# Optimization experiments

Hardware: AMD Instinct MI355X
Metric: run time of the kernel (lower is better)

The kernel has to match this reference:

```python
import jax, jax.numpy as jnp
import numpy as np

EPS = 1e-12  # torch F.normalize eps

def _l2norm(x):
    n = jnp.linalg.norm(x, axis=1, keepdims=True)
    return x / jnp.maximum(n, EPS)

def setup_inputs() -> dict:
    key = jax.random.key(0)
    kq, km = jax.random.split(key)
    queries = jax.random.normal(kq, (4096, 128), dtype=jnp.float32)
    memory = jax.random.normal(km, (100000, 128), dtype=jnp.float32)
    return {"queries": queries, "memory": memory, "k": 3}

def reference(queries, memory, k):
    q = _l2norm(queries)                      # [N, D]
    m = _l2norm(memory)                       # [M, D]
    sims = q @ m.T                            # [N, M]
    values, indices = jax.lax.top_k(sims, k)  # [N, k] each
    distances = 1.0 - values
    return distances, indices
```

## Files before the change

kernel.cpp:

```cpp
#include <hip/hip_runtime.h>
#include <hip/hip_bf16.h>

typedef unsigned short u16;
typedef unsigned int u32;
typedef unsigned long long u64;

#define N_Q 4096
#define N_M 100000
#define N_M_PAD 100096
#define DDIM 128
#define QTILE 256
#define MTILE 64
#define NCHUNK 32
#define NQT (N_Q / QTILE)
#define TOTAL_MT (N_M_PAD / MTILE)
#define TPC ((TOTAL_MT + NCHUNK - 1) / NCHUNK)
#define NCAND (NCHUNK * 2 * 3)

typedef short bf16x8 __attribute__((ext_vector_type(8)));
typedef float f32x4 __attribute__((ext_vector_type(4)));
typedef float f32x16 __attribute__((ext_vector_type(16)));

static __device__ __forceinline__ u16 f2bf(float v) {
  union { float f; u32 u; } a; a.f = v;
  u32 r = a.u + 0x7fffu + ((a.u >> 16) & 1u);
  return (u16)(r >> 16);
}

static __device__ __forceinline__ void async_copy16(const u16* gp, u16* lp) {
  __builtin_amdgcn_global_load_lds(
      (const __attribute__((address_space(1))) u32*)gp,
      (__attribute__((address_space(3))) u32*)lp, 16, 0, 0);
}

static __device__ __forceinline__ int mbcnt64(u64 m) {
  return __builtin_amdgcn_mbcnt_hi((u32)(m >> 32),
                                   __builtin_amdgcn_mbcnt_lo((u32)m, 0));
}

__global__ __launch_bounds__(256) void knorm(const float* __restrict__ q, const float* __restrict__ m,
                                             u16* __restrict__ qn, u16* __restrict__ mn,
                                             float* __restrict__ qinv, float* __restrict__ minv) {
  const int lane = threadIdx.x & 63;
  const int l16 = lane & 15;
  const int sub = lane >> 4;
  const int wgl = blockIdx.x * 4 + (threadIdx.x >> 6);
  const int step = gridDim.x * 16;
  for (int row = wgl * 4 + sub; row < N_Q + N_M_PAD; row += step) {
    const float* src;
    u16* dst;
    int mr = 0;
    bool is_q = (row < N_Q);
    bool pad = false;
    if (is_q) {
      src = q + (size_t)row * DDIM;
      dst = qn + (size_t)row * DDIM;
    } else {
      mr = row - N_Q;
      pad = (mr >= N_M);
      src = m + (size_t)mr * DDIM;
      dst = mn + (size_t)mr * DDIM;
    }
    float4 a, b;
    if (pad) {
      a.x = a.y = a.z = a.w = 0.f;
      b = a;
    } else {
      a = ((const float4*)src)[l16];
      b = ((const float4*)src)[l16 + 16];
    }
    float s = a.x * a.x + a.y * a.y + a.z * a.z + a.w * a.w +
              b.x * b.x + b.y * b.y + b.z * b.z + b.w * b.w;
    #pragma unroll
    for (int off = 1; off < 16; off <<= 1) s += __shfl_xor(s, off, 64);
    float invn = 1.0f / fmaxf(sqrtf(s), 1e-12f);
    u32 p0 = (u32)f2bf(a.x * invn) | ((u32)f2bf(a.y * invn) << 16);
    u32 p1 = (u32)f2bf(a.z * invn) | ((u32)f2bf(a.w * invn) << 16);
    u32 p2 = (u32)f2bf(b.x * invn) | ((u32)f2bf(b.y * invn) << 16);
    u32 p3 = (u32)f2bf(b.z * invn) | ((u32)f2bf(b.w * invn) << 16);
    uint2 w0; w0.x = p0; w0.y = p1;
    uint2 w1; w1.x = p2; w1.y = p3;
    *(uint2*)&dst[l16 * 4] = w0;
    *(uint2*)&dst[64 + l16 * 4] = w1;
    if (l16 == 0) {
      if (is_q) qinv[row] = invn;
      else minv[mr] = pad ? 0.f : invn;
    }
  }
}

static __device__ __forceinline__ void stage2(const u16* __restrict__ mn, u16* dst,
                                              int t, const u32* goff, u32 loff0) {
  const u16* gbase = mn + (size_t)t * MTILE * DDIM;
  #pragma unroll
  for (int it = 0; it < 2; ++it)
    async_copy16(gbase + goff[it], dst + loff0 + (u32)(it * 64) * 8);
}

static __device__ __forceinline__ void tileWork(
    const u16* As, int tl, int wm, int h, int l15, int l31,
    const bf16x8 (&bq)[2][8], float (&tv0)[2], float (&tv1)[2], float (&tv2)[2]) {
  f32x16 acc[2];
  __builtin_amdgcn_s_setprio(1);
  {
    int c = h ^ l15;
    bf16x8 a = *(const bf16x8*)&As[((wm * 32 + l31) * 16 + c) * 8];
    f32x16 z = {0.f,0.f,0.f,0.f,0.f,0.f,0.f,0.f,0.f,0.f,0.f,0.f,0.f,0.f,0.f,0.f};
    acc[0] = __builtin_amdgcn_mfma_f32_32x32x16_bf16(a, bq[0][0], z, 0, 0, 0);
    acc[1] = __builtin_amdgcn_mfma_f32_32x32x16_bf16(a, bq[1][0], z, 0, 0, 0);
  }
  #pragma unroll
  for (int s = 1; s < 8; ++s) {
    int c = (s * 2 + h) ^ l15;
    bf16x8 a = *(const bf16x8*)&As[((wm * 32 + l31) * 16 + c) * 8];
    acc[0] = __builtin_amdgcn_mfma_f32_32x32x16_bf16(a, bq[0][s], acc[0], 0, 0, 0);
    acc[1] = __builtin_amdgcn_mfma_f32_32x32x16_bf16(a, bq[1][s], acc[1], 0, 0, 0);
  }
  __builtin_amdgcn_s_setprio(0);
  const u32 codeBase = ((u32)tl << 2) | ((u32)h << 1);
  #pragma unroll
  for (int ni = 0; ni < 2; ++ni) {
    #pragma unroll
    for (int g = 0; g < 2; ++g) {
      float M = fmaxf(
          fmaxf(fmaxf(acc[ni][g * 8 + 0], acc[ni][g * 8 + 1]),
                fmaxf(acc[ni][g * 8 + 2], acc[ni][g * 8 + 3])),
          fmaxf(fmaxf(acc[ni][g * 8 + 4], acc[ni][g * 8 + 5]),
                fmaxf(acc[ni][g * 8 + 6], acc[ni][g * 8 + 7])));
      float pk = __uint_as_float((__float_as_uint(M) & 0xFFFFFE00u) | (codeBase | (u32)g));
      tv2[ni] = __builtin_amdgcn_fmed3f(tv1[ni], tv2[ni], pk);
      tv1[ni] = __builtin_amdgcn_fmed3f(tv0[ni], tv1[ni], pk);
      tv0[ni] = fmaxf(tv0[ni], pk);
    }
  }
}

__global__ __launch_bounds__(512, 4) void kgemm(const u16* __restrict__ qn,
                                                const u16* __restrict__ mn,
                                                float* __restrict__ pval) {
  __shared__ u16 B0[MTILE * DDIM];
  __shared__ u16 B1[MTILE * DDIM];
  __shared__ u16 B2[MTILE * DDIM];
  __shared__ u16 B3[MTILE * DDIM];

  const int id = blockIdx.x;
  const int xcd = id & 7, sub = id >> 3;
  const int ch = xcd * 4 + (sub >> 4);
  const int qt = sub & 15;
  const int tid = threadIdx.x;
  const int wid = tid >> 6, lane = tid & 63;
  const int l15 = lane & 15, l31 = lane & 31, h = lane >> 5;
  const int wm = wid >> 2, wq = wid & 3;

  const int t0 = ch * TPC;
  const int t1 = (t0 + TPC < TOTAL_MT) ? (t0 + TPC) : TOTAL_MT;
  const int nt = t1 - t0;

  u32 goff[2];
  u32 loff0;
  {
    int u0 = wid * 128 + lane;
    loff0 = (u32)(wid * 128) * 8;
    #pragma unroll
    for (int it = 0; it < 2; ++it) {
      int u = u0 + it * 64;
      int row = u >> 4, su = u & 15;
      int k8 = su ^ (row & 15);
      goff[it] = (u32)(row * DDIM + k8 * 8);
    }
  }

  stage2(mn, B0, t0 + 0, goff, loff0);
  stage2(mn, B1, t0 + 1, goff, loff0);
  stage2(mn, B2, t0 + 2, goff, loff0);

  bf16x8 bq[2][8];
  #pragma unroll
  for (int ni = 0; ni < 2; ++ni) {
    int col = qt * QTILE + wq * 64 + ni * 32 + l31;
    #pragma unroll
    for (int s = 0; s < 8; ++s)
      bq[ni][s] = *(const bf16x8*)&qn[(size_t)col * DDIM + (s * 2 + h) * 8];
  }

  float tv0[2], tv1[2], tv2[2];
  #pragma unroll
  for (int i = 0; i < 2; ++i) { tv0[i] = tv1[i] = tv2[i] = -1e30f; }

  asm volatile("s_waitcnt vmcnt(0)" ::: "memory");
  asm volatile("s_barrier" ::: "memory");

  int r = 0;
  #define ROUND(BC, BS)                                                        \
    {                                                                          \
      int ts = t0 + r + 3;                                                     \
      ts = (ts < t1) ? ts : (t1 - 1);                                          \
      stage2(mn, BS, ts, goff, loff0);                                         \
      tileWork(BC, r, wm, h, l15, l31, bq, tv0, tv1, tv2);                     \
      asm volatile("s_waitcnt vmcnt(4)" ::: "memory");                         \
      asm volatile("s_barrier" ::: "memory");                                  \
      ++r;                                                                     \
      if (r >= nt) break;                                                      \
    }
  while (true) {
    ROUND(B0, B3)
    ROUND(B1, B0)
    ROUND(B2, B1)
    ROUND(B3, B2)
  }
  #undef ROUND

  #pragma unroll
  for (int ni = 0; ni < 2; ++ni) {
    float a0 = tv0[ni], a1 = tv1[ni], a2 = tv2[ni];
    float b0 = __shfl_xor(a0, 32, 64);
    float b1 = __shfl_xor(a1, 32, 64);
    float b2 = __shfl_xor(a2, 32, 64);
    float n0 = fmaxf(a0, b0);
    float n1 = __builtin_amdgcn_fmed3f(a0, b0, fmaxf(a1, b1));
    float n2 = fmaxf(fmaxf(fminf(a1, b0), fminf(a0, b1)), fmaxf(a2, b2));
    int qlocal = wq * 64 + ni * 32 + l31;
    size_t base = (((size_t)qt * NCHUNK + ch) * QTILE + qlocal) * 6 + wm * 3;
    if (h == 0) {
      pval[base] = n0;
      pval[base + 1] = n1;
    } else {
      pval[base + 2] = n2;
    }
  }
}

__global__ __launch_bounds__(256) void kmerge(const float* __restrict__ pval,
                                              const float* __restrict__ q,
                                              const float* __restrict__ mem,
                                              const float* __restrict__ qinv,
                                              const float* __restrict__ minv,
                                              float* __restrict__ out) {
  __shared__ float sv[4][64];
  __shared__ u32 spk[4][8];
  __shared__ u32 spo[4][8];
  const int tid = threadIdx.x;
  const int wq = tid >> 6;
  const int lane = tid & 63;
  const int qg = blockIdx.x * 4 + wq;
  const int qt = qg >> 8, ql = qg & 255;

  const int c0 = lane * 3;
  float cv[3];
  {
    int chn = c0 / 6, rem = c0 - chn * 6;
    size_t b = (((size_t)qt * NCHUNK + chn) * QTILE + ql) * 6 + rem;
    cv[0] = pval[b];
    cv[1] = pval[b + 1];
    cv[2] = pval[b + 2];
  }

  u32 k[3];
  #pragma unroll
  for (int i = 0; i < 3; ++i) {
    u32 u = __float_as_uint(cv[i]);
    k[i] = (u & 0x80000000u) ? ~u : (u | 0x80000000u);
  }

  u32 t = 0;
  #pragma unroll
  for (int b = 31; b >= 0; --b) {
    u32 cand = t | (1u << b);
    int loc = (int)(k[0] >= cand) + (int)(k[1] >= cand) + (int)(k[2] >= cand);
    u64 B0 = __ballot(loc & 1);
    u64 B1 = __ballot(loc & 2);
    int cnt = __popcll(B0) + 2 * __popcll(B1);
    if (cnt >= 8) t = cand;
  }

  {
    u64 G[3], E[3];
    #pragma unroll
    for (int i = 0; i < 3; ++i) {
      G[i] = __ballot(k[i] > t);
      E[i] = __ballot(k[i] == t);
    }
    int c1 = __popcll(G[0]) + __popcll(G[1]) + __popcll(G[2]);
    int bg = mbcnt64(G[0]) + mbcnt64(G[1]) + mbcnt64(G[2]);
    int be = mbcnt64(E[0]) + mbcnt64(E[1]) + mbcnt64(E[2]);
    int og = 0, oe = 0;
    #pragma unroll
    for (int i = 0; i < 3; ++i) {
      int slot = 99;
      if (k[i] > t) { slot = bg + og; ++og; }
      else if (k[i] == t) { slot = c1 + be + oe; ++oe; }
      if (slot < 8) {
        spk[wq][slot] = __float_as_uint(cv[i]);
        spo[wq][slot] = (u32)(c0 + i);
      }
    }
  }
  __syncthreads();

  const float qi = qinv[qg];
  const float* qrow = q + (size_t)qg * DDIM;
  const int e = lane >> 3, f = lane & 7;

  float4 qv[4];
  #pragma unroll
  for (int i = 0; i < 4; ++i) qv[i] = *(const float4*)&qrow[(f + 8 * i) * 4];

  #pragma unroll
  for (int p = 0; p < 8; ++p) {
    int bp = (int)spo[wq][p];
    u32 code = spk[wq][p] & 511u;
    int chn = bp / 6;
    int wm = (bp - chn * 6) / 3;
    int tl = (int)(code >> 2), hh = (int)((code >> 1) & 1u), g = (int)(code & 1u);
    int row = (chn * TPC + tl) * MTILE + wm * 32 + g * 16 + (e >> 2) * 8 + hh * 4 + (e & 3);
    bool valid = (row < N_M);
    int ra = valid ? row : 0;
    const float* mrow = mem + (size_t)ra * DDIM;
    float s = 0.f;
    #pragma unroll
    for (int i = 0; i < 4; ++i) {
      float4 mv = *(const float4*)&mrow[(f + 8 * i) * 4];
      s += qv[i].x * mv.x + qv[i].y * mv.y + qv[i].z * mv.z + qv[i].w * mv.w;
    }
    #pragma unroll
    for (int off = 1; off < 8; off <<= 1) s += __shfl_xor(s, off, 64);
    s = valid ? (s * qi * minv[ra]) : -1e30f;
    if (f == 0) sv[wq][p * 8 + e] = s;
  }
  __syncthreads();

  float myv = sv[wq][lane];
  {
    int p = lane >> 3, e2 = lane & 7;
    int bp = (int)spo[wq][p];
    u32 code = spk[wq][p] & 511u;
    int chn = bp / 6;
    int wm = (bp - chn * 6) / 3;
    int tl = (int)(code >> 2), hh = (int)((code >> 1) & 1u), g = (int)(code & 1u);
    int row = (chn * TPC + tl) * MTILE + wm * 32 + g * 16 + (e2 >> 2) * 8 + hh * 4 + (e2 & 3);
    int myrow = (row < N_M) ? row : (N_M + lane);

    #pragma unroll
    for (int a = 0; a < 3; ++a) {
      float bv = myv; int bi = myrow;
      #pragma unroll
      for (int off = 32; off >= 1; off >>= 1) {
        float ov = __shfl_xor(bv, off, 64);
        int oi = __shfl_xor(bi, off, 64);
        bool g2 = (ov > bv) || (ov == bv && oi < bi);
        bv = g2 ? ov : bv; bi = g2 ? oi : bi;
      }
      if (lane == 0) {
        out[(size_t)qg * 3 + a] = 1.0f - bv;
        out[(size_t)N_Q * 3 + (size_t)qg * 3 + a] = (float)bi;
      }
      if (myrow == bi) myv = -1e31f;
    }
  }
}

extern "C" void kernel_launch(void* const* d_in, const int* in_sizes, int n_in,
                              void* d_out, int out_size, void* d_ws, size_t ws_size,
                              hipStream_t stream) {
  const float* q = (const float*)d_in[0];
  const float* m = (const float*)d_in[1];

  char* ws = (char*)d_ws;
  size_t off = 0;
  u16* qn = (u16*)(ws + off); off += (size_t)N_Q * DDIM * 2;
  u16* mn = (u16*)(ws + off); off += (size_t)N_M_PAD * DDIM * 2;
  float* qinv = (float*)(ws + off); off += (size_t)N_Q * 4;
  float* minv = (float*)(ws + off); off += (size_t)N_M_PAD * 4;
  float* pval = (float*)(ws + off); off += (size_t)N_Q * NCAND * 4;

  knorm<<<1024, 256, 0, stream>>>(q, m, qn, mn, qinv, minv);
  kgemm<<<NQT * NCHUNK, 512, 0, stream>>>(qn, mn, pval);
  kmerge<<<N_Q / 4, 256, 0, stream>>>(pval, q, m, qinv, minv, (float*)d_out);
}
```

Measured before the change: 201.1 us.

## Split memory into 48 chunks with triple-buffered LDS and widen merge

Raises the number of memory chunks from 32 to 48, so the GEMM grid has more blocks and each block processes fewer tiles. To fit more blocks per CU, the LDS ring shrinks from four to three buffers with a prefetch distance of two tiles. The merge kernel now reads six candidates per lane from the first 48 lanes and pads the remaining lanes with sentinels. The trade-off is less latency hiding per block and more partial candidates to merge.

```diff
diff --git a/kernel.cpp b/kernel.cpp
--- a/kernel.cpp
+++ b/kernel.cpp
@@ -11,7 +11,7 @@
 #define DDIM 128
 #define QTILE 256
 #define MTILE 64
-#define NCHUNK 32
+#define NCHUNK 48
 #define NQT (N_Q / QTILE)
 #define TOTAL_MT (N_M_PAD / MTILE)
 #define TPC ((TOTAL_MT + NCHUNK - 1) / NCHUNK)
@@ -141,11 +141,10 @@
   __shared__ u16 B0[MTILE * DDIM];
   __shared__ u16 B1[MTILE * DDIM];
   __shared__ u16 B2[MTILE * DDIM];
-  __shared__ u16 B3[MTILE * DDIM];
 
   const int id = blockIdx.x;
   const int xcd = id & 7, sub = id >> 3;
-  const int ch = xcd * 4 + (sub >> 4);
+  const int ch = xcd * 6 + (sub >> 4);
   const int qt = sub & 15;
   const int tid = threadIdx.x;
   const int wid = tid >> 6, lane = tid & 63;
@@ -172,7 +171,6 @@
 
   stage2(mn, B0, t0 + 0, goff, loff0);
   stage2(mn, B1, t0 + 1, goff, loff0);
-  stage2(mn, B2, t0 + 2, goff, loff0);
 
   bf16x8 bq[2][8];
   #pragma unroll
@@ -193,20 +191,19 @@
   int r = 0;
   #define ROUND(BC, BS)                                                        \
     {                                                                          \
-      int ts = t0 + r + 3;                                                     \
+      int ts = t0 + r + 2;                                                     \
       ts = (ts < t1) ? ts : (t1 - 1);                                          \
       stage2(mn, BS, ts, goff, loff0);                                         \
       tileWork(BC, r, wm, h, l15, l31, bq, tv0, tv1, tv2);                     \
-      asm volatile("s_waitcnt vmcnt(4)" ::: "memory");                         \
+      asm volatile("s_waitcnt vmcnt(2)" ::: "memory");                         \
       asm volatile("s_barrier" ::: "memory");                                  \
       ++r;                                                                     \
       if (r >= nt) break;                                                      \
     }
   while (true) {
-    ROUND(B0, B3)
+    ROUND(B0, B2)
     ROUND(B1, B0)
     ROUND(B2, B1)
-    ROUND(B3, B2)
   }
   #undef ROUND
 
@@ -245,19 +242,19 @@
   const int qg = blockIdx.x * 4 + wq;
   const int qt = qg >> 8, ql = qg & 255;
 
-  const int c0 = lane * 3;
-  float cv[3];
-  {
-    int chn = c0 / 6, rem = c0 - chn * 6;
-    size_t b = (((size_t)qt * NCHUNK + chn) * QTILE + ql) * 6 + rem;
-    cv[0] = pval[b];
-    cv[1] = pval[b + 1];
-    cv[2] = pval[b + 2];
-  }
-
-  u32 k[3];
-  #pragma unroll
-  for (int i = 0; i < 3; ++i) {
+  const int c0 = lane * 6;
+  float cv[6];
+  #pragma unroll
+  for (int i = 0; i < 6; ++i) cv[i] = -1e31f;
+  if (lane < NCHUNK) {
+    size_t b = (((size_t)qt * NCHUNK + lane) * QTILE + ql) * 6;
+    #pragma unroll
+    for (int i = 0; i < 6; ++i) cv[i] = pval[b + i];
+  }
+
+  u32 k[6];
+  #pragma unroll
+  for (int i = 0; i < 6; ++i) {
     u32 u = __float_as_uint(cv[i]);
     k[i] = (u & 0x80000000u) ? ~u : (u | 0x80000000u);
   }
@@ -266,26 +263,33 @@
   #pragma unroll
   for (int b = 31; b >= 0; --b) {
     u32 cand = t | (1u << b);
-    int loc = (int)(k[0] >= cand) + (int)(k[1] >= cand) + (int)(k[2] >= cand);
-    u64 B0 = __ballot(loc & 1);
-    u64 B1 = __ballot(loc & 2);
-    int cnt = __popcll(B0) + 2 * __popcll(B1);
+    int loc = 0;
+    #pragma unroll
+    for (int i = 0; i < 6; ++i) loc += (int)(k[i] >= cand);
+    u64 M0 = __ballot(loc & 1);
+    u64 M1 = __ballot(loc & 2);
+    u64 M2 = __ballot(loc & 4);
+    int cnt = __popcll(M0) + 2 * __popcll(M1) + 4 * __popcll(M2);
     if (cnt >= 8) t = cand;
   }
 
   {
-    u64 G[3], E[3];
-    #pragma unroll
-    for (int i = 0; i < 3; ++i) {
+    u64 G[6], E[6];
+    #pragma unroll
+    for (int i = 0; i < 6; ++i) {
       G[i] = __ballot(k[i] > t);
       E[i] = __ballot(k[i] == t);
     }
-    int c1 = __popcll(G[0]) + __popcll(G[1]) + __popcll(G[2]);
-    int bg = mbcnt64(G[0]) + mbcnt64(G[1]) + mbcnt64(G[2]);
-    int be = mbcnt64(E[0]) + mbcnt64(E[1]) + mbcnt64(E[2]);
+    int c1 = 0, bg = 0, be = 0;
+    #pragma unroll
+    for (int i = 0; i < 6; ++i) {
+      c1 += __popcll(G[i]);
+      bg += mbcnt64(G[i]);
+      be += mbcnt64(E[i]);
+    }
     int og = 0, oe = 0;
     #pragma unroll
-    for (int i = 0; i < 3; ++i) {
+    for (int i = 0; i < 6; ++i) {
       int slot = 99;
       if (k[i] > t) { slot = bg + og; ++og; }
       else if (k[i] == t) { slot = c1 + be + oe; ++oe; }
```

Measured after the change: 207.0 us. 2.9% more time.
